# Optimization experiments

Hardware: AMD Instinct MI355X
Metric: run time of the kernel (lower is better)

Reference implementation:

```python
import jax, jax.numpy as jnp
import numpy as np

V, D = 100000, 300          # fastText vocab / dim
CV, CD, L = 128, 16, 16     # char vocab / char emb dim / word length
F = 50                      # filters per kernel
KS = (3, 4, 5)              # char CNN kernel widths
H = 150                     # LSTM hidden per direction (2H == D)
FH = 150                    # alpha-encoder FFNN hidden
NF, FE = 64, 50             # entity feature vocab / dim
A = 2000                    # num actors
T = 1024                    # tokens
E = 512                     # entity spans
MAXSPAN = 10                # max span length (ragged -> padded+masked)


def setup_inputs() -> dict:
    key = jax.random.key(0)
    ks = jax.random.split(key, 24)
    g = lambda i, shape, s=0.05: jax.random.normal(ks[i], shape, jnp.float32) * s
    inp = {}
    inp['fast_text'] = g(0, (V, D), 0.1)
    inp['actor_matrix'] = g(1, (A, D), 0.1)
    inp['char_table'] = g(2, (CV, CD), 0.1)
    for j, k in enumerate(KS):
        inp[f'conv_w{k}'] = g(3 + j, (F, CD, k))
        inp[f'conv_b{k}'] = jnp.zeros((F,), jnp.float32)
    din = D + F * len(KS)  # 450 = fastText + char features
    inp['Wi_f'] = g(6, (4 * H, din)); inp['Wh_f'] = g(7, (4 * H, H)); inp['b_f'] = jnp.zeros((4 * H,), jnp.float32)
    inp['Wi_b'] = g(8, (4 * H, din)); inp['Wh_b'] = g(9, (4 * H, H)); inp['b_b'] = jnp.zeros((4 * H,), jnp.float32)
    inp['alpha_W1'] = g(10, (D, FH)); inp['alpha_b1'] = jnp.zeros((FH,), jnp.float32)
    inp['alpha_W2'] = g(11, (FH, FH)); inp['alpha_b2'] = jnp.zeros((FH,), jnp.float32)
    inp['alpha_w_out'] = g(12, (FH,))
    inp['feat_table'] = g(13, (NF, FE), 0.1)
    span_dim = 3 * D + 2 * FE  # 1000, per Model1.span_encoding_dim
    inp['affine_W'] = g(14, (span_dim, D)); inp['affine_b'] = jnp.zeros((D,), jnp.float32)
    inp['word_ids'] = jax.random.randint(ks[15], (T,), 0, V)
    inp['char_ids'] = jax.random.randint(ks[16], (T, L), 0, CV)
    starts = jax.random.randint(ks[17], (E,), 0, T - MAXSPAN)
    lens = jax.random.randint(ks[18], (E,), 1, MAXSPAN + 1)
    feats = jax.random.randint(ks[19], (E, 2), 0, NF)
    inp['espans'] = jnp.concatenate([starts[:, None], (starts + lens)[:, None], feats], axis=1)
    return inp


def _renorm(e):
    # nn.Embedding(max_norm=1.0): renormalize looked-up rows to L2 norm <= 1
    n = jnp.linalg.norm(e, axis=-1, keepdims=True)
    return e * jnp.minimum(1.0, 1.0 / jnp.maximum(n, 1e-7))


def _lstm(x, Wi, Wh, b, reverse):
    Hh = Wh.shape[1]
    def step(carry, xt):
        h, c = carry
        z = xt @ Wi.T + h @ Wh.T + b
        i, f, g2, o = jnp.split(z, 4)
        i = jax.nn.sigmoid(i); f = jax.nn.sigmoid(f)
        g2 = jnp.tanh(g2); o = jax.nn.sigmoid(o)
        c = f * c + i * g2
        h = o * jnp.tanh(c)
        return (h, c), h
    init = (jnp.zeros((Hh,), x.dtype), jnp.zeros((Hh,), x.dtype))
    _, hs = jax.lax.scan(step, init, x, reverse=reverse)
    return hs  # [T, H], hs[i] corresponds to position i


def reference(fast_text, actor_matrix, char_table, conv_w3, conv_b3, conv_w4, conv_b4,
              conv_w5, conv_b5, Wi_f, Wh_f, b_f, Wi_b, Wh_b, b_b,
              alpha_W1, alpha_b1, alpha_W2, alpha_b2, alpha_w_out,
              feat_table, affine_W, affine_b, word_ids, char_ids, espans):
    # --- WordEncoder: fastText + char CNN -> BiLSTM contextual embeddings ---
    ft = fast_text[word_ids]                       # [T, D] fastText embeddings (values)
    ce = char_table[char_ids]                      # [T, L, CD]
    xc = jnp.transpose(ce, (0, 2, 1))              # [T, CD, L]
    feats = []
    for w, bb in ((conv_w3, conv_b3), (conv_w4, conv_b4), (conv_w5, conv_b5)):
        y = jax.lax.conv_general_dilated(xc, w, (1,), 'VALID',
                                         dimension_numbers=('NCW', 'OIW', 'NCW'))
        feats.append(jnp.max(jax.nn.relu(y + bb[None, :, None]), axis=-1))  # [T, F]
    char_feat = jnp.concatenate(feats, axis=-1)    # [T, 150]
    lstm_in = jnp.concatenate([ft, char_feat], axis=-1)  # [T, 450]
    h_f = _lstm(lstm_in, Wi_f, Wh_f, b_f, False)
    h_b = _lstm(lstm_in, Wi_b, Wh_b, b_b, True)
    keys = jnp.concatenate([h_f, h_b], axis=-1)    # [T, D] contextual word embeddings
    values = ft

    # --- espan_encodings: ragged span gather, padded + masked, fully vectorized ---
    s, e = espans[:, 0], espans[:, 1]
    fidx = espans[:, 2:]                           # [E, 2]
    offs = jnp.arange(MAXSPAN)
    idx = jnp.clip(s[:, None] + offs[None, :], 0, keys.shape[0] - 1)  # [E, S]
    mask = offs[None, :] < (e - s)[:, None]        # [E, S]
    k_sp = keys[idx]                               # [E, S, D]
    v_sp = values[idx]                             # [E, S, D]
    # SingleQueryEncoder (alpha_encoder): FFNN scores over keys, softmax-pool values
    hsc = jax.nn.relu(k_sp @ alpha_W1 + alpha_b1)
    hsc = jax.nn.relu(hsc @ alpha_W2 + alpha_b2)
    logits = jnp.where(mask, hsc @ alpha_w_out, -1e30)  # [E, S]
    attn = jax.nn.softmax(logits, axis=-1)
    xh = jnp.einsum('es,esd->ed', attn, v_sp)      # [E, D]
    xf = keys[s]                                   # first token
    xl = keys[e - 1]                               # last token
    fs = _renorm(feat_table[fidx]).reshape(fidx.shape[0], -1)  # [E, 2*FE]
    enc = jnp.concatenate([xf, xl, xh, fs], axis=-1)  # [E, 3D+2FE]

    small = enc @ affine_W + affine_b              # [E, D] affine_ent
    actors = _renorm(actor_matrix)                 # [A, D] actor_embedding max_norm=1
    score_link = actors @ small.T                  # [A, E] DotProduct.simpel
    score_1 = jax.nn.logsumexp(score_link, axis=1) # [A]   Maximum.lse over dim=1
    return score_1, score_link
```

## Files before the change

### kernel.cpp

```cpp
#include <hip/hip_runtime.h>
#include <math.h>

typedef _Float16 h2f __attribute__((ext_vector_type(2)));

__device__ __forceinline__ float fdot2f(h2f a, h2f b, float c) {
#if __has_builtin(__builtin_amdgcn_fdot2)
  return __builtin_amdgcn_fdot2(a, b, c, false);
#else
  return c + (float)a[0] * (float)b[0] + (float)a[1] * (float)b[1];
#endif
}

__device__ __forceinline__ float sigf(float x) {
  return __builtin_amdgcn_rcpf(1.f + __expf(-x));
}
__device__ __forceinline__ float tanh_fast(float x) {
  return 2.f * __builtin_amdgcn_rcpf(1.f + __expf(-2.f * x)) - 1.f;
}

__device__ __forceinline__ int clampi(int v, int lo, int hi) {
  return v < lo ? lo : (v > hi ? hi : v);
}

__global__ __launch_bounds__(64) void k_token(
    const float* __restrict__ fast_text, const float* __restrict__ char_table,
    const float* __restrict__ w3, const float* __restrict__ b3,
    const float* __restrict__ w4, const float* __restrict__ b4,
    const float* __restrict__ w5, const float* __restrict__ b5,
    const int* __restrict__ word_ids, const int* __restrict__ char_ids,
    float* __restrict__ lstm_in) {
  const int t = blockIdx.x;
  const int tid = threadIdx.x;
  __shared__ float ce[16][16];
  for (int i = tid; i < 256; i += 64) {
    int l = i >> 4, ci = i & 15;
    ce[l][ci] = char_table[char_ids[t * 16 + l] * 16 + ci];
  }
  __syncthreads();
  const int wid = word_ids[t];
  for (int d = tid; d < 300; d += 64)
    lstm_in[t * 450 + d] = fast_text[wid * 300 + d];
  const int f = tid;
  if (f < 50) {
    {
      float acc[14];
#pragma unroll
      for (int p = 0; p < 14; ++p) acc[p] = 0.f;
      for (int ci = 0; ci < 16; ++ci) {
#pragma unroll
        for (int kk = 0; kk < 3; ++kk) {
          float wv = w3[(f * 16 + ci) * 3 + kk];
#pragma unroll
          for (int p = 0; p < 14; ++p) acc[p] += ce[p + kk][ci] * wv;
        }
      }
      float m = acc[0];
#pragma unroll
      for (int p = 1; p < 14; ++p) m = fmaxf(m, acc[p]);
      lstm_in[t * 450 + 300 + f] = fmaxf(0.f, m + b3[f]);
    }
    {
      float acc[13];
#pragma unroll
      for (int p = 0; p < 13; ++p) acc[p] = 0.f;
      for (int ci = 0; ci < 16; ++ci) {
#pragma unroll
        for (int kk = 0; kk < 4; ++kk) {
          float wv = w4[(f * 16 + ci) * 4 + kk];
#pragma unroll
          for (int p = 0; p < 13; ++p) acc[p] += ce[p + kk][ci] * wv;
        }
      }
      float m = acc[0];
#pragma unroll
      for (int p = 1; p < 13; ++p) m = fmaxf(m, acc[p]);
      lstm_in[t * 450 + 350 + f] = fmaxf(0.f, m + b4[f]);
    }
    {
      float acc[12];
#pragma unroll
      for (int p = 0; p < 12; ++p) acc[p] = 0.f;
      for (int ci = 0; ci < 16; ++ci) {
#pragma unroll
        for (int kk = 0; kk < 5; ++kk) {
          float wv = w5[(f * 16 + ci) * 5 + kk];
#pragma unroll
          for (int p = 0; p < 12; ++p) acc[p] += ce[p + kk][ci] * wv;
        }
      }
      float m = acc[0];
#pragma unroll
      for (int p = 1; p < 12; ++p) m = fmaxf(m, acc[p]);
      lstm_in[t * 450 + 400 + f] = fmaxf(0.f, m + b5[f]);
    }
  }
}

__global__ __launch_bounds__(256) void gemm_nt(
    const float* __restrict__ A, const float* __restrict__ W,
    const float* __restrict__ bias, float* __restrict__ C,
    int M, int N, int K) {
  __shared__ float As[16][64];
  __shared__ float Ws[16][64];
  const int tid = threadIdx.x;
  const int tx = tid & 15, ty = tid >> 4;
  const int r0 = blockIdx.x * 64, c0 = blockIdx.y * 64;
  float acc[4][4] = {};
  for (int k0 = 0; k0 < K; k0 += 16) {
    for (int i = tid; i < 1024; i += 256) {
      int rr = i >> 4, kk = i & 15;
      int r = r0 + rr, k = k0 + kk;
      As[kk][rr] = (r < M && k < K) ? A[r * K + k] : 0.f;
      int c = c0 + rr;
      Ws[kk][rr] = (c < N && k < K) ? W[c * K + k] : 0.f;
    }
    __syncthreads();
#pragma unroll
    for (int kk = 0; kk < 16; ++kk) {
      const float4 av = *(const float4*)(&As[kk][ty * 4]);
      const float4 wv = *(const float4*)(&Ws[kk][tx * 4]);
      float a[4] = {av.x, av.y, av.z, av.w};
      float w[4] = {wv.x, wv.y, wv.z, wv.w};
#pragma unroll
      for (int i = 0; i < 4; ++i)
#pragma unroll
        for (int j = 0; j < 4; ++j) acc[i][j] += a[i] * w[j];
    }
    __syncthreads();
  }
#pragma unroll
  for (int i = 0; i < 4; ++i) {
    int r = r0 + ty * 4 + i;
    if (r >= M) continue;
#pragma unroll
    for (int j = 0; j < 4; ++j) {
      int c = c0 + tx * 4 + j;
      if (c < N) C[r * N + c] = acc[i][j] + (bias ? bias[c] : 0.f);
    }
  }
}

__attribute__((amdgpu_waves_per_eu(3, 3)))
__global__ __launch_bounds__(640) void k_lstm(
    const float* __restrict__ xprojF, const float* __restrict__ xprojB,
    const float* __restrict__ Wh_f, const float* __restrict__ Wh_b,
    float* __restrict__ keys) {
  const int dir = blockIdx.x;
  const float* __restrict__ xp = dir ? xprojB : xprojF;
  const float* __restrict__ Wh = dir ? Wh_b : Wh_f;
  const int tid = threadIdx.x;
  const int u = tid >> 2;
  const int g = tid & 3;
  const int row = g * 150 + u;
  const bool act = (tid < 600);

  __shared__ alignas(16) h2f hbuf[2][76];

  h2f w[75];
  if (act) {
    const float2* Wr = (const float2*)(Wh + row * 150);
#pragma unroll
    for (int kk = 0; kk < 75; ++kk) {
      float2 a = Wr[kk];
      h2f v;
      v[0] = (_Float16)a.x;
      v[1] = (_Float16)a.y;
      w[kk] = v;
    }
  }
  for (int i = tid; i < 152; i += 640) {
    h2f z;
    z[0] = (_Float16)0.f;
    z[1] = (_Float16)0.f;
    hbuf[i / 76][i % 76] = z;
  }
  float c = 0.f;
  float xv = act ? xp[(dir ? 1023 : 0) * 600 + row] : 0.f;
  __syncthreads();

  int cur = 0;
  for (int step = 0; step < 1024; ++step) {
    const int t = dir ? (1023 - step) : step;
    const int tn = dir ? (t > 0 ? t - 1 : 0) : (t < 1023 ? t + 1 : 1023);
    float z = 0.f;
    if (act) {
      const float xv_next = xp[tn * 600 + row];
      const float4* hv = (const float4*)hbuf[cur];
      float a0 = 0.f, a1 = 0.f, a2 = 0.f, a3 = 0.f;
#pragma unroll
      for (int cidx = 0; cidx < 18; ++cidx) {
        float4 q = hv[cidx];
        const h2f* hh = (const h2f*)&q;
        a0 = fdot2f(w[4 * cidx + 0], hh[0], a0);
        a1 = fdot2f(w[4 * cidx + 1], hh[1], a1);
        a2 = fdot2f(w[4 * cidx + 2], hh[2], a2);
        a3 = fdot2f(w[4 * cidx + 3], hh[3], a3);
      }
      {
        float4 q = hv[18];
        const h2f* hh = (const h2f*)&q;
        a0 = fdot2f(w[72], hh[0], a0);
        a1 = fdot2f(w[73], hh[1], a1);
        a2 = fdot2f(w[74], hh[2], a2);
      }
      z = (a0 + a1) + (a2 + a3) + xv;
      xv = xv_next;
    }
    float val = 0.f;
    if (act) {
      const float zz = (g == 2) ? 2.f * z : z;
      const float s = sigf(zz);
      val = (g == 2) ? (2.f * s - 1.f) : s;
    }
    const float v1 = __shfl_xor(val, 1);
    const float gv = __shfl_xor(val, 2);
    const float ov = __shfl_xor(v1, 2);
    if (act && g == 0) {
      c = v1 * c + val * gv;
      const float h = ov * tanh_fast(c);
      keys[t * 300 + dir * 150 + u] = h;
      ((_Float16*)hbuf[cur ^ 1])[u] = (_Float16)h;
    }
    cur ^= 1;
    __syncthreads();
  }
}

__global__ __launch_bounds__(320) void k_span(
    const float* __restrict__ keys, const float* __restrict__ lstm_in,
    const float* __restrict__ W1, const float* __restrict__ b1,
    const float* __restrict__ W2, const float* __restrict__ b2,
    const float* __restrict__ w_out, const float* __restrict__ feat_table,
    const int* __restrict__ espans, float* __restrict__ enc) {
  const int e = blockIdx.x;
  const int tid = threadIdx.x;
  const int s = espans[e * 4 + 0];
  const int en = espans[e * 4 + 1];
  const int f0 = espans[e * 4 + 2];
  const int f1 = espans[e * 4 + 3];

  __shared__ float ksh[10][300];
  __shared__ float hsh[10][152];
  __shared__ float h2sh[10][152];
  __shared__ float att[10];
  __shared__ float scl[2];

  for (int i = tid; i < 3000; i += 320) {
    int p = i / 300, d = i % 300;
    int row = clampi(s + p, 0, 1023);
    ksh[p][d] = keys[row * 300 + d];
  }
  __syncthreads();

  if (tid < 152) {
    int jj = tid;
    if (jj < 150) {
      float acc[10];
#pragma unroll
      for (int p = 0; p < 10; ++p) acc[p] = b1[jj];
      for (int k = 0; k < 300; k += 4) {
        float w0 = W1[(k + 0) * 150 + jj];
        float w1 = W1[(k + 1) * 150 + jj];
        float w2 = W1[(k + 2) * 150 + jj];
        float w3 = W1[(k + 3) * 150 + jj];
#pragma unroll
        for (int p = 0; p < 10; ++p) {
          const float4 kv = *(const float4*)(&ksh[p][k]);
          acc[p] += kv.x * w0 + kv.y * w1 + kv.z * w2 + kv.w * w3;
        }
      }
#pragma unroll
      for (int p = 0; p < 10; ++p) hsh[p][jj] = fmaxf(acc[p], 0.f);
    } else {
#pragma unroll
      for (int p = 0; p < 10; ++p) hsh[p][jj] = 0.f;
    }
  }
  __syncthreads();

  if (tid < 150) {
    int jj = tid;
    float acc[10];
#pragma unroll
    for (int p = 0; p < 10; ++p) acc[p] = b2[jj];
    for (int k = 0; k < 152; k += 4) {
      float w0 = (k + 0 < 150) ? W2[(k + 0) * 150 + jj] : 0.f;
      float w1 = (k + 1 < 150) ? W2[(k + 1) * 150 + jj] : 0.f;
      float w2 = (k + 2 < 150) ? W2[(k + 2) * 150 + jj] : 0.f;
      float w3 = (k + 3 < 150) ? W2[(k + 3) * 150 + jj] : 0.f;
#pragma unroll
      for (int p = 0; p < 10; ++p) {
        const float4 hv = *(const float4*)(&hsh[p][k]);
        acc[p] += hv.x * w0 + hv.y * w1 + hv.z * w2 + hv.w * w3;
      }
    }
#pragma unroll
    for (int p = 0; p < 10; ++p) h2sh[p][jj] = fmaxf(acc[p], 0.f);
  }
  __syncthreads();

  if (tid < 10) {
    float lg = -1e30f;
    if (tid < en - s) {
      float d = 0.f;
      for (int k = 0; k < 150; ++k) d += h2sh[tid][k] * w_out[k];
      lg = d;
    }
    att[tid] = lg;
  }
  if (tid >= 64 && tid < 66) {
    int r = tid - 64;
    int fi = (r == 0) ? f0 : f1;
    float nsq = 0.f;
    for (int k = 0; k < 50; ++k) {
      float v = feat_table[fi * 50 + k];
      nsq += v * v;
    }
    float n = sqrtf(nsq);
    scl[r] = fminf(1.f, 1.f / fmaxf(n, 1e-7f));
  }
  __syncthreads();

  if (tid == 0) {
    float m = -1e30f;
    for (int p = 0; p < 10; ++p) m = fmaxf(m, att[p]);
    float ex[10];
    float ssum = 0.f;
    for (int p = 0; p < 10; ++p) {
      ex[p] = expf(att[p] - m);
      ssum += ex[p];
    }
    for (int p = 0; p < 10; ++p) att[p] = ex[p] / ssum;
  }
  __syncthreads();

  if (tid < 300) {
    int d = tid;
    float xf = keys[s * 300 + d];
    float xl = keys[(en - 1) * 300 + d];
    float xh = 0.f;
#pragma unroll
    for (int p = 0; p < 10; ++p) {
      int row = clampi(s + p, 0, 1023);
      xh += att[p] * lstm_in[row * 450 + d];
    }
    enc[e * 1000 + d] = xf;
    enc[e * 1000 + 300 + d] = xl;
    enc[e * 1000 + 600 + d] = xh;
  }
  if (tid < 100) {
    int r = tid / 50, cc = tid % 50;
    int fi = (r == 0) ? f0 : f1;
    enc[e * 1000 + 900 + tid] = feat_table[fi * 50 + cc] * scl[r];
  }
}

__global__ __launch_bounds__(320) void k_affine(
    const float* __restrict__ enc, const float* __restrict__ W,
    const float* __restrict__ bias, float* __restrict__ small) {
  const int e0 = blockIdx.x * 4;
  const int tid = threadIdx.x;
  __shared__ float es[4][1000];
  for (int i = tid; i < 4000; i += 320) es[i / 1000][i % 1000] = enc[e0 * 1000 + i];
  __syncthreads();
  if (tid < 300) {
    float a0 = bias[tid], a1 = bias[tid], a2 = bias[tid], a3 = bias[tid];
    for (int k = 0; k < 1000; k += 4) {
      float w0 = W[(k + 0) * 300 + tid];
      float w1 = W[(k + 1) * 300 + tid];
      float w2 = W[(k + 2) * 300 + tid];
      float w3 = W[(k + 3) * 300 + tid];
      const float4 v0 = *(const float4*)(&es[0][k]);
      const float4 v1 = *(const float4*)(&es[1][k]);
      const float4 v2 = *(const float4*)(&es[2][k]);
      const float4 v3 = *(const float4*)(&es[3][k]);
      a0 += v0.x * w0 + v0.y * w1 + v0.z * w2 + v0.w * w3;
      a1 += v1.x * w0 + v1.y * w1 + v1.z * w2 + v1.w * w3;
      a2 += v2.x * w0 + v2.y * w1 + v2.z * w2 + v2.w * w3;
      a3 += v3.x * w0 + v3.y * w1 + v3.z * w2 + v3.w * w3;
    }
    small[(e0 + 0) * 300 + tid] = a0;
    small[(e0 + 1) * 300 + tid] = a1;
    small[(e0 + 2) * 300 + tid] = a2;
    small[(e0 + 3) * 300 + tid] = a3;
  }
}

__global__ __launch_bounds__(64) void k_renorm(
    const float* __restrict__ actors, float* __restrict__ actorsN) {
  const int a = blockIdx.x;
  const int l = threadIdx.x;
  float nsq = 0.f;
  for (int d = l; d < 300; d += 64) {
    float v = actors[a * 300 + d];
    nsq += v * v;
  }
  for (int off = 32; off; off >>= 1) nsq += __shfl_down(nsq, off);
  nsq = __shfl(nsq, 0);
  float sc = fminf(1.f, 1.f / fmaxf(sqrtf(nsq), 1e-7f));
  for (int d = l; d < 300; d += 64) actorsN[a * 300 + d] = actors[a * 300 + d] * sc;
}

__global__ __launch_bounds__(64) void k_lse(
    const float* __restrict__ link, float* __restrict__ out) {
  const int a = blockIdx.x;
  const int l = threadIdx.x;
  float v[8];
  float m = -1e30f;
#pragma unroll
  for (int i = 0; i < 8; ++i) {
    v[i] = link[a * 512 + l + i * 64];
    m = fmaxf(m, v[i]);
  }
  for (int off = 32; off; off >>= 1) m = fmaxf(m, __shfl_xor(m, off));
  float ssum = 0.f;
#pragma unroll
  for (int i = 0; i < 8; ++i) ssum += expf(v[i] - m);
  for (int off = 32; off; off >>= 1) ssum += __shfl_xor(ssum, off);
  if (l == 0) out[a] = logf(ssum) + m;
}

extern "C" void kernel_launch(void* const* d_in, const int* in_sizes, int n_in,
                              void* d_out, int out_size, void* d_ws, size_t ws_size,
                              hipStream_t stream) {
  const float* fast_text = (const float*)d_in[0];
  const float* actor_matrix = (const float*)d_in[1];
  const float* char_table = (const float*)d_in[2];
  const float* w3 = (const float*)d_in[3];
  const float* b3 = (const float*)d_in[4];
  const float* w4 = (const float*)d_in[5];
  const float* b4 = (const float*)d_in[6];
  const float* w5 = (const float*)d_in[7];
  const float* b5 = (const float*)d_in[8];
  const float* Wi_f = (const float*)d_in[9];
  const float* Wh_f = (const float*)d_in[10];
  const float* b_f = (const float*)d_in[11];
  const float* Wi_b = (const float*)d_in[12];
  const float* Wh_b = (const float*)d_in[13];
  const float* b_b = (const float*)d_in[14];
  const float* alpha_W1 = (const float*)d_in[15];
  const float* alpha_b1 = (const float*)d_in[16];
  const float* alpha_W2 = (const float*)d_in[17];
  const float* alpha_b2 = (const float*)d_in[18];
  const float* alpha_w_out = (const float*)d_in[19];
  const float* feat_table = (const float*)d_in[20];
  const float* affine_W = (const float*)d_in[21];
  const float* affine_b = (const float*)d_in[22];
  const int* word_ids = (const int*)d_in[23];
  const int* char_ids = (const int*)d_in[24];
  const int* espans = (const int*)d_in[25];

  float* ws = (float*)d_ws;
  float* lstm_in = ws;
  float* xpF = lstm_in + 460800;
  float* xpB = xpF + 614400;
  float* keys = xpB + 614400;
  float* enc = keys + 307200;
  float* small = enc + 512000;
  float* actN = small + 153600;

  float* out = (float*)d_out;
  float* score_link = out + 2000;

  k_token<<<1024, 64, 0, stream>>>(fast_text, char_table, w3, b3, w4, b4, w5, b5,
                                   word_ids, char_ids, lstm_in);
  gemm_nt<<<dim3(16, 10), 256, 0, stream>>>(lstm_in, Wi_f, b_f, xpF, 1024, 600, 450);
  gemm_nt<<<dim3(16, 10), 256, 0, stream>>>(lstm_in, Wi_b, b_b, xpB, 1024, 600, 450);
  k_lstm<<<2, 640, 0, stream>>>(xpF, xpB, Wh_f, Wh_b, keys);
  k_renorm<<<2000, 64, 0, stream>>>(actor_matrix, actN);
  k_span<<<512, 320, 0, stream>>>(keys, lstm_in, alpha_W1, alpha_b1, alpha_W2,
                                  alpha_b2, alpha_w_out, feat_table, espans, enc);
  k_affine<<<128, 320, 0, stream>>>(enc, affine_W, affine_b, small);
  gemm_nt<<<dim3(32, 8), 256, 0, stream>>>(actN, small, nullptr, score_link,
                                           2000, 512, 300);
  k_lse<<<2000, 64, 0, stream>>>(score_link, out);
}
```

Before: 1.237 ms.

## Split LSTM recurrent dot across quad lanes and reduce with DPP

Each lane of a 4-lane group now holds a 40-column slice of all four gate rows for its hidden unit, instead of one full 150-wide gate row. It accumulates four partial dot products, and the group combines them with DPP quad-permute adds. The old ds_bpermute shuffles for gate exchange are also replaced by DPP moves. Each lane now reads only 5 float4s of h from shared memory instead of 19, which shortens the per-step LDS read and FMA chain on the serial 1024-step critical path. The cost is a few extra cross-lane reductions and selects per step.

```diff
diff --git a/kernel.cpp b/kernel.cpp
--- a/kernel.cpp
+++ b/kernel.cpp
@@ -9,6 +9,14 @@
 #else
   return c + (float)a[0] * (float)b[0] + (float)a[1] * (float)b[1];
 #endif
+}
+
+template <int CTRL>
+__device__ __forceinline__ float dpp_f(float x) {
+  union { float f; int i; } u, r;
+  u.f = x;
+  r.i = __builtin_amdgcn_update_dpp(0, u.i, CTRL, 0xF, 0xF, false);
+  return r.f;
 }
 
 __device__ __forceinline__ float sigf(float x) {
@@ -154,25 +162,34 @@
   const int row = g * 150 + u;
   const bool act = (tid < 600);
 
-  __shared__ alignas(16) h2f hbuf[2][76];
-
-  h2f w[75];
+  __shared__ alignas(16) h2f hbuf[2][80];
+
+  h2f w[4][20];
   if (act) {
-    const float2* Wr = (const float2*)(Wh + row * 150);
-#pragma unroll
-    for (int kk = 0; kk < 75; ++kk) {
-      float2 a = Wr[kk];
-      h2f v;
-      v[0] = (_Float16)a.x;
-      v[1] = (_Float16)a.y;
-      w[kk] = v;
-    }
-  }
-  for (int i = tid; i < 152; i += 640) {
+#pragma unroll
+    for (int j = 0; j < 4; ++j) {
+      const float* Wr = Wh + (j * 150 + u) * 150;
+#pragma unroll
+      for (int kk = 0; kk < 20; ++kk) {
+        const int k = 40 * g + 2 * kk;
+        float x0 = 0.f, x1 = 0.f;
+        if (k < 150) {
+          const float2 p = *(const float2*)(Wr + k);
+          x0 = p.x;
+          x1 = p.y;
+        }
+        h2f v;
+        v[0] = (_Float16)x0;
+        v[1] = (_Float16)x1;
+        w[j][kk] = v;
+      }
+    }
+  }
+  for (int i = tid; i < 160; i += 640) {
     h2f z;
     z[0] = (_Float16)0.f;
     z[1] = (_Float16)0.f;
-    hbuf[i / 76][i % 76] = z;
+    hbuf[i / 80][i % 80] = z;
   }
   float c = 0.f;
   float xv = act ? xp[(dir ? 1023 : 0) * 600 + row] : 0.f;
@@ -182,44 +199,44 @@
   for (int step = 0; step < 1024; ++step) {
     const int t = dir ? (1023 - step) : step;
     const int tn = dir ? (t > 0 ? t - 1 : 0) : (t < 1023 ? t + 1 : 1023);
-    float z = 0.f;
     if (act) {
       const float xv_next = xp[tn * 600 + row];
-      const float4* hv = (const float4*)hbuf[cur];
+      const float4* hv = (const float4*)hbuf[cur] + 5 * g;
       float a0 = 0.f, a1 = 0.f, a2 = 0.f, a3 = 0.f;
 #pragma unroll
-      for (int cidx = 0; cidx < 18; ++cidx) {
-        float4 q = hv[cidx];
+      for (int i = 0; i < 5; ++i) {
+        float4 q = hv[i];
         const h2f* hh = (const h2f*)&q;
-        a0 = fdot2f(w[4 * cidx + 0], hh[0], a0);
-        a1 = fdot2f(w[4 * cidx + 1], hh[1], a1);
-        a2 = fdot2f(w[4 * cidx + 2], hh[2], a2);
-        a3 = fdot2f(w[4 * cidx + 3], hh[3], a3);
-      }
-      {
-        float4 q = hv[18];
-        const h2f* hh = (const h2f*)&q;
-        a0 = fdot2f(w[72], hh[0], a0);
-        a1 = fdot2f(w[73], hh[1], a1);
-        a2 = fdot2f(w[74], hh[2], a2);
-      }
-      z = (a0 + a1) + (a2 + a3) + xv;
+#pragma unroll
+        for (int m = 0; m < 4; ++m) {
+          a0 = fdot2f(w[0][4 * i + m], hh[m], a0);
+          a1 = fdot2f(w[1][4 * i + m], hh[m], a1);
+          a2 = fdot2f(w[2][4 * i + m], hh[m], a2);
+          a3 = fdot2f(w[3][4 * i + m], hh[m], a3);
+        }
+      }
+      const float e0 = a0 + dpp_f<0xB1>(a0);
+      const float e1 = a1 + dpp_f<0xB1>(a1);
+      const float e2 = a2 + dpp_f<0xB1>(a2);
+      const float e3 = a3 + dpp_f<0xB1>(a3);
+      const float fa = (g & 1) ? e1 : e0;
+      const float fb = (g & 1) ? e3 : e2;
+      const float ga_ = fa + dpp_f<0x4E>(fa);
+      const float gb_ = fb + dpp_f<0x4E>(fb);
+      const float z = ((g & 2) ? gb_ : ga_) + xv;
       xv = xv_next;
-    }
-    float val = 0.f;
-    if (act) {
       const float zz = (g == 2) ? 2.f * z : z;
       const float s = sigf(zz);
-      val = (g == 2) ? (2.f * s - 1.f) : s;
-    }
-    const float v1 = __shfl_xor(val, 1);
-    const float gv = __shfl_xor(val, 2);
-    const float ov = __shfl_xor(v1, 2);
-    if (act && g == 0) {
-      c = v1 * c + val * gv;
-      const float h = ov * tanh_fast(c);
-      keys[t * 300 + dir * 150 + u] = h;
-      ((_Float16*)hbuf[cur ^ 1])[u] = (_Float16)h;
+      const float val = (g == 2) ? (2.f * s - 1.f) : s;
+      const float v1 = dpp_f<0xB1>(val);
+      const float gv = dpp_f<0x4E>(val);
+      const float ov = dpp_f<0x4E>(v1);
+      if (g == 0) {
+        c = v1 * c + val * gv;
+        const float h = ov * tanh_fast(c);
+        keys[t * 300 + dir * 150 + u] = h;
+        ((_Float16*)hbuf[cur ^ 1])[u] = (_Float16)h;
+      }
     }
     cur ^= 1;
     __syncthreads();
```

Measured after the change: 1.233 ms. Within noise of the previous version (-0.3%).
